# Optimization experiments

Measured on AMD Instinct MI355X. Metric: run time of the kernel, lower is better.

## Reference

```python
import jax, jax.numpy as jnp
import numpy as np

SIZES = (20, 20, 20, 20, 20)          # formula_oh_sizes
OH_N = sum(SIZES)                      # 100
NUM_BINS = 65536                       # spect_bin.get_num_bins()
EPS_SIZE = 1e-4                        # eps added to subset size
IN_EPS = 1e-5                          # torch InstanceNorm1d default eps


def thermometer_oh(counts):
    # StructuredOneHot with accum=True: per-element thermometer encoding.
    # counts: (N, E) element counts -> (N, sum(SIZES)) with out[j]=1 iff j < count.
    outs = [(jnp.arange(s, dtype=counts.dtype)[None, :] < counts[:, i:i + 1]).astype(jnp.float32)
            for i, s in enumerate(SIZES)]
    return jnp.concatenate(outs, axis=-1)


def inorm(x):
    # InstanceNorm1d (affine=False) as applied here: normalize over last dim per row.
    m = jnp.mean(x, axis=-1, keepdims=True)
    v = jnp.var(x, axis=-1, keepdims=True)
    return (x - m) * jax.lax.rsqrt(v + IN_EPS)


def _lin(key, fan_in, fan_out):
    k1, k2 = jax.random.split(key)
    bound = 1.0 / np.sqrt(fan_in)
    W = jax.random.uniform(k1, (fan_in, fan_out), jnp.float32, -bound, bound)
    b = jax.random.uniform(k2, (fan_out,), jnp.float32, -bound, bound)
    return W, b


def setup_inputs():
    key = jax.random.key(0)
    ks = jax.random.split(key, 12)
    B, A, GF, S, P, E, D = 8, 48, 256, 4096, 32, 5, 256
    vert_feat_in = jax.random.normal(ks[0], (B, A, GF), jnp.float32)
    vert_mask_in = jnp.ones((B, A), jnp.float32)
    elem_idx = jax.random.randint(ks[1], (B, A), 0, E)
    vert_element_oh = jax.nn.one_hot(elem_idx, E, dtype=jnp.float32)
    adj_oh = jnp.zeros((B, A, A), jnp.float32)                      # unused by forward path
    atom_subsets = jax.random.randint(ks[2], (B, S, A), 0, 2).astype(jnp.int32)
    atom_subsets_peaks = jnp.zeros((1,), jnp.float32)               # unused (mass_idx/intensity used)
    mass_idx = jax.random.randint(ks[3], (B, S, P), 0, NUM_BINS).astype(jnp.int32)
    intensity = jax.random.uniform(ks[4], (B, S, P), jnp.float32)
    combine_W, combine_b = _lin(ks[5], OH_N + GF, GF)
    l1_W, l1_b = _lin(ks[6], GF, D)
    l2a_W, l2a_b = _lin(ks[7], D, D)
    l2b_W, l2b_b = _lin(ks[8], D, D)
    score_W, score_b = _lin(ks[9], D, 1)
    return {
        'vert_feat_in': vert_feat_in, 'vert_mask_in': vert_mask_in,
        'vert_element_oh': vert_element_oh, 'adj_oh': adj_oh,
        'atom_subsets': atom_subsets, 'atom_subsets_peaks': atom_subsets_peaks,
        'mass_idx': mass_idx, 'intensity': intensity,
        'combine_W': combine_W, 'combine_b': combine_b,
        'l1_W': l1_W, 'l1_b': l1_b, 'l2a_W': l2a_W, 'l2a_b': l2a_b,
        'l2b_W': l2b_W, 'l2b_b': l2b_b, 'score_W': score_W, 'score_b': score_b,
    }


def reference(vert_feat_in, vert_mask_in, vert_element_oh, adj_oh, atom_subsets,
              atom_subsets_peaks, mass_idx, intensity,
              combine_W, combine_b, l1_W, l1_b, l2a_W, l2a_b, l2b_W, l2b_b,
              score_W, score_b):
    B, A, GF = vert_feat_in.shape
    _, S, _ = atom_subsets.shape
    subsets_f = atom_subsets.astype(jnp.float32)
    masked_vert = vert_feat_in * vert_mask_in[:, :, None]               # (B,A,GF)
    subsets_masked = subsets_f * vert_mask_in[:, None, :]               # (B,S,A)
    # weighted sum of vertex features over each subset
    sws = jnp.einsum('bag,bsa->bsg', masked_vert, subsets_masked)        # (B,S,GF)
    # per-subset element counts -> structured one-hot formula encoding
    counts = jnp.einsum('bae,bsa->bse', vert_element_oh, subsets_f)      # (B,S,E)
    pf_oh = thermometer_oh(counts.reshape(-1, counts.shape[-1])).reshape(B, S, OH_N)
    subset_size = jnp.sum(subsets_masked, axis=2) + EPS_SIZE             # (B,S)
    mean_feat = sws / subset_size[:, :, None]
    normed = inorm(mean_feat)                                            # subset_weighted_norm
    combined = jax.nn.relu(jnp.concatenate([pf_oh, normed], -1) @ combine_W + combine_b)
    x = inorm(combined)                                                  # norm_post_combine
    x = jax.nn.relu(x @ l1_W + l1_b)
    x = jax.nn.leaky_relu(x @ l2a_W + l2a_b)
    x = jax.nn.leaky_relu(x @ l2b_W + l2b_b)
    x = jax.nn.relu(x)
    x = inorm(x)                                                         # norm_pre_score
    scores = (x @ score_W + score_b)[..., 0]                             # (B,S)
    probs = jax.nn.softmax(scores, axis=-1)
    # per-batch sparse mass-matrix binning: scatter-add intensity*prob into spectral bins
    weighted = intensity * probs[:, :, None]                             # (B,S,P)
    seg = jax.vmap(lambda idx, w: jax.ops.segment_sum(w, idx, num_segments=NUM_BINS))
    spect_out = seg(mass_idx.reshape(B, -1), weighted.reshape(B, -1))    # (B,NUM_BINS)
    return spect_out, probs
```

## Files before the change

### kernel.cpp

```cpp
#include <hip/hip_runtime.h>
#include <math.h>

#define B_DIM 8
#define A_DIM 48
#define GF_DIM 256
#define S_DIM 4096
#define P_DIM 32
#define E_DIM 5
#define OHN 100
#define NBINS 65536

typedef __attribute__((ext_vector_type(8))) short short8v;
typedef __attribute__((ext_vector_type(4))) float float4v;

__device__ __forceinline__ float wave_sum(float v) {
#pragma unroll
    for (int o = 32; o; o >>= 1) v += __shfl_xor(v, o, 64);
    return v;
}
__device__ __forceinline__ float wave_max(float v) {
#pragma unroll
    for (int o = 32; o; o >>= 1) v = fmaxf(v, __shfl_xor(v, o, 64));
    return v;
}
__device__ __forceinline__ float quad16_sum(float v) {
    v += __shfl_xor(v, 1, 64); v += __shfl_xor(v, 2, 64);
    v += __shfl_xor(v, 4, 64); v += __shfl_xor(v, 8, 64);
    return v;
}
__device__ __forceinline__ unsigned short bf16_rn(float x) {
    unsigned int u = __float_as_uint(x);
    return (unsigned short)((u + 0x7FFFu + ((u >> 16) & 1u)) >> 16);
}
__device__ __forceinline__ float bf16_val(unsigned short h) {
    return __uint_as_float(((unsigned int)h) << 16);
}
__device__ __forceinline__ float4v mfma_bf16(short8v a, short8v b, float4v c) {
    return __builtin_amdgcn_mfma_f32_16x16x32_bf16(a, b, c, 0, 0, 0);
}

__global__ __launch_bounds__(256) void k_prep(
    const float* __restrict__ cW, const float* __restrict__ l1W,
    const float* __restrict__ l2aW, const float* __restrict__ l2bW,
    const float* __restrict__ vert_feat, const float* __restrict__ vert_mask,
    const float* __restrict__ elem_oh,
    short* __restrict__ wp, short* __restrict__ wv,
    float* __restrict__ maskB, int* __restrict__ eiB,
    float4* __restrict__ spect4)
{
    const int blk = blockIdx.x;
    const int tid = threadIdx.x;
    if (blk < 1152) {
        int e = blk * 256 + tid;
        int c = e >> 13;
        int i = e & 8191;
        int j    = i & 7;
        int lane = (i >> 3) & 63;
        int nt   = (i >> 9) & 1;
        int wn   = i >> 10;
        int krel = (lane >> 4) * 8 + j;
        int n    = wn * 32 + nt * 16 + (lane & 15);
        float val = 0.f;
        if (c < 12) {
            int kp = c * 32 + krel;
            if (kp < 100)       val = cW[kp * 256 + n];
            else if (kp >= 128) val = cW[(kp - 28) * 256 + n];
        } else {
            int L  = (c - 12) >> 3;
            int kc = (c - 12) & 7;
            const float* W = (L == 0) ? l1W : (L == 1) ? l2aW : l2bW;
            val = W[(kc * 32 + krel) * 256 + n];
        }
        unsigned short h = bf16_rn(val);
        float lo = val - bf16_val(h);
        int base = c * 16384 + (i & 511);
        wp[base + (wn * 4 + nt) * 512]     = (short)h;
        wp[base + (wn * 4 + 2 + nt) * 512] = (short)bf16_rn(lo);
    } else if (blk < 1664) {
        int vb = blk - 1152;
        int vc = vb >> 5;
        int i  = (vb & 31) * 256 + tid;
        int b  = vc >> 1, v = vc & 1;
        int j    = i & 7;
        int lane = (i >> 3) & 63;
        int nt   = (i >> 9) & 1;
        int wn   = i >> 10;
        int k = v * 32 + (lane >> 4) * 8 + j;
        int n = wn * 32 + nt * 16 + (lane & 15);
        float val = 0.f;
        if (k < A_DIM) {
            float mk = vert_mask[b * A_DIM + k];
            val = vert_feat[((size_t)(b * A_DIM + k)) * GF_DIM + n] * mk * mk;
        }
        unsigned short h = bf16_rn(val);
        float lo = val - bf16_val(h);
        int base = vc * 16384 + (i & 511);
        wv[base + (wn * 4 + nt) * 512]     = (short)h;
        wv[base + (wn * 4 + 2 + nt) * 512] = (short)bf16_rn(lo);
    } else if (blk == 1664) {
        for (int t = tid; t < B_DIM * A_DIM; t += 256) {
            maskB[t] = vert_mask[t];
            int ei = 0;
#pragma unroll
            for (int e = 0; e < E_DIM; ++e)
                if (elem_oh[t * E_DIM + e] > 0.5f) ei = e;
            eiB[t] = ei;
        }
    } else {
        int z = (blk - 1665) * 256 + tid;
        spect4[z] = make_float4(0.f, 0.f, 0.f, 0.f);
    }
}

#define L_XAL 16384
#define L_PS  32768
#define L_TM  34816
#define L_INV 35328
#define L_TOT 35456

template <int NKC, int ACT, bool NORM, bool SCORE, bool THERM>
__device__ __forceinline__ void layer_pass(
    short* xAh, short* xAl, float (*ps)[64], const uint4* __restrict__ tm,
    const short* __restrict__ wstream, const float* __restrict__ bias,
    const float* __restrict__ sW, const float* __restrict__ sb,
    float* __restrict__ scores, int R0)
{
    const int tid  = threadIdx.x;
    const int lane = tid & 63;
    const int wn   = tid >> 6;
    const int quad = lane >> 4;
    const int col  = lane & 15;
    const short* wbase = wstream + wn * 2048 + lane * 8;

    unsigned int tw01 = 0, tw23 = 0;
    if (THERM) {
        const int sh = quad * 8;
        uint4 t0 = tm[col];
        uint4 t1 = tm[16 + col];
        tw01 = ((t0.x >> sh) & 0xFFu)        | (((t1.x >> sh) & 0xFFu) << 8)
             | (((t0.y >> sh) & 0xFFu) << 16) | (((t1.y >> sh) & 0xFFu) << 24);
        tw23 = ((t0.z >> sh) & 0xFFu)        | (((t1.z >> sh) & 0xFFu) << 8)
             | (((t0.w >> sh) & 0xFFu) << 16) | (((t1.w >> sh) & 0xFFu) << 24);
    }

    float4v acc[2][2];
#pragma unroll
    for (int mi = 0; mi < 2; ++mi)
#pragma unroll
        for (int nt = 0; nt < 2; ++nt) acc[mi][nt] = (float4v){0.f, 0.f, 0.f, 0.f};

    short8v bh[2][2], bl[2][2];
    {
        const short* q = wbase;
        bh[0][0] = *(const short8v*)(q);
        bh[0][1] = *(const short8v*)(q + 512);
        bl[0][0] = *(const short8v*)(q + 1024);
        bl[0][1] = *(const short8v*)(q + 1536);
    }

#pragma unroll
    for (int kc = 0; kc < NKC; ++kc) {
        const int cur = kc & 1;
        if (kc + 1 < NKC) {
            const int nxt = (kc + 1) & 1;
            const short* q = wbase + (kc + 1) * 16384;
            bh[nxt][0] = *(const short8v*)(q);
            bh[nxt][1] = *(const short8v*)(q + 512);
            bl[nxt][0] = *(const short8v*)(q + 1024);
            bl[nxt][1] = *(const short8v*)(q + 1536);
        }
        const bool isT = THERM && (kc < 4);
        short8v ah[2], al[2];
        if (isT) {
            const unsigned int w = (kc < 2) ? tw01 : tw23;
#pragma unroll
            for (int mi = 0; mi < 2; ++mi) {
                const int bb = (kc & 1) * 16 + mi * 8;
                short8v hv;
#pragma unroll
                for (int j = 0; j < 8; ++j)
                    hv[j] = (short)(((w >> (bb + j)) & 1u) ? 0x3F80 : 0);
                ah[mi] = hv;
            }
        } else {
            const int ki = THERM ? (kc - 4) : kc;
#pragma unroll
            for (int mi = 0; mi < 2; ++mi) {
                ah[mi] = *(const short8v*)(xAh + ((ki * 2 + mi) * 64 + lane) * 8);
                al[mi] = *(const short8v*)(xAl + ((ki * 2 + mi) * 64 + lane) * 8);
            }
        }
#pragma unroll
        for (int mi = 0; mi < 2; ++mi)
#pragma unroll
            for (int nt = 0; nt < 2; ++nt) {
                acc[mi][nt] = mfma_bf16(ah[mi], bh[cur][nt], acc[mi][nt]);
                acc[mi][nt] = mfma_bf16(ah[mi], bl[cur][nt], acc[mi][nt]);
                if (!isT)
                    acc[mi][nt] = mfma_bf16(al[mi], bh[cur][nt], acc[mi][nt]);
            }
    }

    float bc0 = bias[wn * 32 + col];
    float bc1 = bias[wn * 32 + 16 + col];
#pragma unroll
    for (int mi = 0; mi < 2; ++mi)
#pragma unroll
        for (int r = 0; r < 4; ++r) {
            float z0 = acc[mi][0][r] + bc0;
            float z1 = acc[mi][1][r] + bc1;
            if (ACT == 0) { z0 = fmaxf(z0, 0.f); z1 = fmaxf(z1, 0.f); }
            else { z0 = (z0 > 0.f) ? z0 : 0.01f * z0; z1 = (z1 > 0.f) ? z1 : 0.01f * z1; }
            acc[mi][0][r] = z0; acc[mi][1][r] = z1;
        }

    __syncthreads();

    if (NORM) {
#pragma unroll
        for (int mi = 0; mi < 2; ++mi)
#pragma unroll
            for (int r = 0; r < 4; ++r) {
                float s  = acc[mi][0][r] + acc[mi][1][r];
                float s2 = acc[mi][0][r] * acc[mi][0][r]
                         + acc[mi][1][r] * acc[mi][1][r];
                s  = quad16_sum(s);
                s2 = quad16_sum(s2);
                if (col == 0) {
                    ps[wn][mi * 16 + quad * 4 + r]      = s;
                    ps[wn][32 + mi * 16 + quad * 4 + r] = s2;
                }
            }
        __syncthreads();
#pragma unroll
        for (int mi = 0; mi < 2; ++mi)
#pragma unroll
            for (int r = 0; r < 4; ++r) {
                int m = mi * 16 + quad * 4 + r;
                float s = 0.f, s2 = 0.f;
#pragma unroll
                for (int w = 0; w < 8; ++w) { s += ps[w][m]; s2 += ps[w][32 + m]; }
                float mean = s * (1.f / 256.f);
                float var  = s2 * (1.f / 256.f) - mean * mean;
                float rsf  = 1.0f / sqrtf(var + 1e-5f);
                acc[mi][0][r] = (acc[mi][0][r] - mean) * rsf;
                acc[mi][1][r] = (acc[mi][1][r] - mean) * rsf;
            }
    }

    if (SCORE) {
        __syncthreads();
        float sv0 = sW[wn * 32 + col];
        float sv1 = sW[wn * 32 + 16 + col];
        float psu[2][4];
#pragma unroll
        for (int mi = 0; mi < 2; ++mi)
#pragma unroll
            for (int r = 0; r < 4; ++r)
                psu[mi][r] = quad16_sum(acc[mi][0][r] * sv0 + acc[mi][1][r] * sv1);
        if (col == 0) {
#pragma unroll
            for (int mi = 0; mi < 2; ++mi)
#pragma unroll
                for (int r = 0; r < 4; ++r)
                    ps[wn][mi * 16 + quad * 4 + r] = psu[mi][r];
        }
        __syncthreads();
        if (tid < 32) {
            float s = sb[0];
#pragma unroll
            for (int w = 0; w < 8; ++w) s += ps[w][tid];
            scores[R0 + tid] = s;
        }
    } else {
#pragma unroll
        for (int mi = 0; mi < 2; ++mi)
#pragma unroll
            for (int nt = 0; nt < 2; ++nt) {
                int nn0 = (nt * 16 + col) & ~1;
                int q2  = nn0 >> 3;
                int j0  = nn0 & 7;
#pragma unroll
                for (int r = 0; r < 4; ++r) {
                    float v  = acc[mi][nt][r];
                    float pv = __shfl_xor(v, 1, 64);
                    int m15 = quad * 4 + r;
                    int rowidx = (wn * 2 + mi) * 64 + q2 * 16 + m15;
                    if ((col & 1) == 0) {
                        unsigned int wd = (unsigned int)bf16_rn(v)
                                        | ((unsigned int)bf16_rn(pv) << 16);
                        ((unsigned int*)xAh)[rowidx * 4 + (j0 >> 1)] = wd;
                    } else {
                        float ls = v  - bf16_val(bf16_rn(v));
                        float lp = pv - bf16_val(bf16_rn(pv));
                        unsigned int wd = (unsigned int)bf16_rn(lp)
                                        | ((unsigned int)bf16_rn(ls) << 16);
                        ((unsigned int*)xAl)[rowidx * 4 + (j0 >> 1)] = wd;
                    }
                }
            }
        __syncthreads();
    }
}

__global__ __launch_bounds__(512, 4) void k_mlp(
    const int* __restrict__ subsets, const short* __restrict__ wprep,
    const short* __restrict__ vertB,
    const float* __restrict__ maskB, const int* __restrict__ eiB,
    const float* __restrict__ cb,  const float* __restrict__ l1b,
    const float* __restrict__ l2ab, const float* __restrict__ l2bb,
    const float* __restrict__ sW,  const float* __restrict__ sb,
    float* __restrict__ scores)
{
    __shared__ __align__(16) char smem[L_TOT];
    short*  xAh = (short*)smem;
    short*  xAl = (short*)(smem + L_XAL);
    short*  fm  = (short*)(smem + L_XAL);
    float (*ps)[64]  = (float(*)[64])(smem + L_PS);
    uint4*  tm       = (uint4*)(smem + L_TM);
    float*  invsz    = (float*)(smem + L_INV);

    const int tid  = threadIdx.x;
    const int lane = tid & 63;
    const int wn   = tid >> 6;
    const int quad = lane >> 4;
    const int col  = lane & 15;
    const int fb   = blockIdx.x;
    const int b    = fb >> 7;
    const int R0   = fb * 32;

    if (tid < 256) {
        int g  = tid;
        int lg = g & 63;
        int t2 = g >> 6;
        int kc = t2 >> 1, mi = t2 & 1;
        int m  = mi * 16 + (lg & 15);
        int k0 = kc * 32 + (lg >> 4) * 8;
        const int* srow = subsets + (size_t)(R0 + m) * A_DIM;
        short8v hv;
#pragma unroll
        for (int j = 0; j < 8; ++j) {
            int k = k0 + j;
            hv[j] = (short)((k < A_DIM && srow[k]) ? 0x3F80 : 0);
        }
        *(short8v*)(fm + g * 8) = hv;
    }

    {
        const float mymask = (lane < A_DIM) ? maskB[b * A_DIM + lane] : 0.f;
        const int   myei   = (lane < A_DIM) ? eiB[b * A_DIM + lane]   : -1;
        unsigned long long* tmw = (unsigned long long*)tm;
#pragma unroll
        for (int i = 0; i < 4; ++i) {
            int r = wn * 4 + i;
            int fl = (lane < A_DIM) ? subsets[(size_t)(R0 + r) * A_DIM + lane] : 0;
            unsigned long long m0 = __ballot(fl != 0 && myei == 0);
            unsigned long long m1 = __ballot(fl != 0 && myei == 1);
            unsigned long long m2 = __ballot(fl != 0 && myei == 2);
            unsigned long long m3 = __ballot(fl != 0 && myei == 3);
            unsigned long long m4 = __ballot(fl != 0 && myei == 4);
            float ssz = wave_sum(fl ? mymask : 0.f) + 1e-4f;
            if (lane == 0) {
                unsigned int c0 = __popcll(m0), c1 = __popcll(m1),
                             c2 = __popcll(m2), c3 = __popcll(m3),
                             c4 = __popcll(m4);
                unsigned long long r0 = (1ull << (c0 > 20u ? 20u : c0)) - 1ull;
                unsigned long long r1 = (1ull << (c1 > 20u ? 20u : c1)) - 1ull;
                unsigned long long r2 = (1ull << (c2 > 20u ? 20u : c2)) - 1ull;
                unsigned long long r3 = (1ull << (c3 > 20u ? 20u : c3)) - 1ull;
                unsigned long long r4 = (1ull << (c4 > 20u ? 20u : c4)) - 1ull;
                unsigned long long lo = r0 | (r1 << 20) | (r2 << 40) | (r3 << 60);
                unsigned long long hi = (r3 >> 4) | (r4 << 16);
                tmw[r * 2]     = lo;
                tmw[r * 2 + 1] = hi;
                invsz[r]  = 1.0f / ssz;
            }
        }
    }
    __syncthreads();

    {
        const short* wbase = vertB + b * 32768 + wn * 2048 + lane * 8;
        float4v acc[2][2];
#pragma unroll
        for (int mi = 0; mi < 2; ++mi)
#pragma unroll
            for (int nt = 0; nt < 2; ++nt) acc[mi][nt] = (float4v){0.f, 0.f, 0.f, 0.f};

        short8v bh[2][2], bl[2][2];
#pragma unroll
        for (int kc = 0; kc < 2; ++kc) {
            const short* q = wbase + kc * 16384;
            bh[kc][0] = *(const short8v*)(q);
            bh[kc][1] = *(const short8v*)(q + 512);
            bl[kc][0] = *(const short8v*)(q + 1024);
            bl[kc][1] = *(const short8v*)(q + 1536);
        }
#pragma unroll
        for (int kc = 0; kc < 2; ++kc) {
            short8v a0 = *(const short8v*)(fm + ((kc * 2 + 0) * 64 + lane) * 8);
            short8v a1 = *(const short8v*)(fm + ((kc * 2 + 1) * 64 + lane) * 8);
#pragma unroll
            for (int nt = 0; nt < 2; ++nt) {
                acc[0][nt] = mfma_bf16(a0, bh[kc][nt], acc[0][nt]);
                acc[0][nt] = mfma_bf16(a0, bl[kc][nt], acc[0][nt]);
                acc[1][nt] = mfma_bf16(a1, bh[kc][nt], acc[1][nt]);
                acc[1][nt] = mfma_bf16(a1, bl[kc][nt], acc[1][nt]);
            }
        }

#pragma unroll
        for (int mi = 0; mi < 2; ++mi)
#pragma unroll
            for (int r = 0; r < 4; ++r) {
                float iv = invsz[mi * 16 + quad * 4 + r];
                acc[mi][0][r] *= iv;
                acc[mi][1][r] *= iv;
            }

        __syncthreads();

        {
#pragma unroll
            for (int mi = 0; mi < 2; ++mi)
#pragma unroll
                for (int r = 0; r < 4; ++r) {
                    float s  = acc[mi][0][r] + acc[mi][1][r];
                    float s2 = acc[mi][0][r] * acc[mi][0][r]
                             + acc[mi][1][r] * acc[mi][1][r];
                    s  = quad16_sum(s);
                    s2 = quad16_sum(s2);
                    if (col == 0) {
                        ps[wn][mi * 16 + quad * 4 + r]      = s;
                        ps[wn][32 + mi * 16 + quad * 4 + r] = s2;
                    }
                }
            __syncthreads();
#pragma unroll
            for (int mi = 0; mi < 2; ++mi)
#pragma unroll
                for (int r = 0; r < 4; ++r) {
                    int m = mi * 16 + quad * 4 + r;
                    float s = 0.f, s2 = 0.f;
#pragma unroll
                    for (int w = 0; w < 8; ++w) { s += ps[w][m]; s2 += ps[w][32 + m]; }
                    float mean = s * (1.f / 256.f);
                    float var  = s2 * (1.f / 256.f) - mean * mean;
                    float rsf  = 1.0f / sqrtf(var + 1e-5f);
                    acc[mi][0][r] = (acc[mi][0][r] - mean) * rsf;
                    acc[mi][1][r] = (acc[mi][1][r] - mean) * rsf;
                }
        }

#pragma unroll
        for (int mi = 0; mi < 2; ++mi)
#pragma unroll
            for (int nt = 0; nt < 2; ++nt) {
                int nn0 = (nt * 16 + col) & ~1;
                int q2  = nn0 >> 3;
                int j0  = nn0 & 7;
#pragma unroll
                for (int r = 0; r < 4; ++r) {
                    float v  = acc[mi][nt][r];
                    float pv = __shfl_xor(v, 1, 64);
                    int m15 = quad * 4 + r;
                    int rowidx = (wn * 2 + mi) * 64 + q2 * 16 + m15;
                    if ((col & 1) == 0) {
                        unsigned int wd = (unsigned int)bf16_rn(v)
                                        | ((unsigned int)bf16_rn(pv) << 16);
                        ((unsigned int*)xAh)[rowidx * 4 + (j0 >> 1)] = wd;
                    } else {
                        float ls = v  - bf16_val(bf16_rn(v));
                        float lp = pv - bf16_val(bf16_rn(pv));
                        unsigned int wd = (unsigned int)bf16_rn(lp)
                                        | ((unsigned int)bf16_rn(ls) << 16);
                        ((unsigned int*)xAl)[rowidx * 4 + (j0 >> 1)] = wd;
                    }
                }
            }
        __syncthreads();
    }

    layer_pass<12, 0, true,  false, true >(xAh, xAl, ps, tm, wprep,
        cb, nullptr, nullptr, nullptr, R0);
    layer_pass< 8, 0, false, false, false>(xAh, xAl, ps, tm, wprep + 12 * 16384,
        l1b, nullptr, nullptr, nullptr, R0);
    layer_pass< 8, 1, false, false, false>(xAh, xAl, ps, tm, wprep + 20 * 16384,
        l2ab, nullptr, nullptr, nullptr, R0);
    layer_pass< 8, 0, true,  true,  false>(xAh, xAl, ps, tm, wprep + 28 * 16384,
        l2bb, sW, sb, scores, R0);
}

__global__ __launch_bounds__(256) void k_softmax(float* __restrict__ probs) {
    const int b   = blockIdx.x;
    const int tid = threadIdx.x;
    __shared__ float redA[4];
    __shared__ float redB[4];
    float* sp = probs + (size_t)b * S_DIM;

    float v[16];
    float mx = -INFINITY;
#pragma unroll
    for (int i = 0; i < 16; ++i) {
        v[i] = sp[tid + i * 256];
        mx = fmaxf(mx, v[i]);
    }
    mx = wave_max(mx);
    if ((tid & 63) == 0) redA[tid >> 6] = mx;
    __syncthreads();
    mx = fmaxf(fmaxf(redA[0], redA[1]), fmaxf(redA[2], redA[3]));

    float sum = 0.f;
#pragma unroll
    for (int i = 0; i < 16; ++i) {
        v[i] = expf(v[i] - mx);
        sum += v[i];
    }
    sum = wave_sum(sum);
    if ((tid & 63) == 0) redB[tid >> 6] = sum;
    __syncthreads();
    float tot = redB[0] + redB[1] + redB[2] + redB[3];
    float inv = 1.0f / tot;
#pragma unroll
    for (int i = 0; i < 16; ++i) sp[tid + i * 256] = v[i] * inv;
}

__global__ __launch_bounds__(256) void k_scatter(
    const int*   __restrict__ mass_idx,
    const float* __restrict__ intensity,
    const float* __restrict__ probs,
    float* __restrict__ spect)
{
    int i  = blockIdx.x * 256 + threadIdx.x;
    int bs = i >> 5;
    int b  = i >> 17;
    float w = intensity[i] * probs[bs];
    unsafeAtomicAdd(spect + ((size_t)b << 16) + mass_idx[i], w);
}

extern "C" void kernel_launch(void* const* d_in, const int* in_sizes, int n_in,
                              void* d_out, int out_size, void* d_ws, size_t ws_size,
                              hipStream_t stream) {
    const float* vert_feat = (const float*)d_in[0];
    const float* vert_mask = (const float*)d_in[1];
    const float* elem_oh   = (const float*)d_in[2];
    const int*   subsets   = (const int*)d_in[4];
    const int*   mass_idx  = (const int*)d_in[6];
    const float* intensity = (const float*)d_in[7];
    const float* combine_W = (const float*)d_in[8];
    const float* combine_b = (const float*)d_in[9];
    const float* l1_W      = (const float*)d_in[10];
    const float* l1_b      = (const float*)d_in[11];
    const float* l2a_W     = (const float*)d_in[12];
    const float* l2a_b     = (const float*)d_in[13];
    const float* l2b_W     = (const float*)d_in[14];
    const float* l2b_b     = (const float*)d_in[15];
    const float* score_W   = (const float*)d_in[16];
    const float* score_b   = (const float*)d_in[17];

    float* out   = (float*)d_out;
    float* spect = out;
    float* probs = out + (size_t)B_DIM * NBINS;

    short* wprep = (short*)d_ws;
    short* vertB = wprep + 36 * 16384;
    float* maskB = (float*)(vertB + 16 * 16384);
    int*   eiB   = (int*)(maskB + B_DIM * A_DIM);

    k_prep<<<2177, 256, 0, stream>>>(combine_W, l1_W, l2a_W, l2b_W,
        vert_feat, vert_mask, elem_oh, wprep, vertB, maskB, eiB,
        (float4*)spect);
    k_mlp<<<1024, 512, 0, stream>>>(subsets, wprep, vertB, maskB, eiB,
        combine_b, l1_b, l2a_b, l2b_b, score_W, score_b, probs);
    k_softmax<<<B_DIM, 256, 0, stream>>>(probs);
    k_scatter<<<(B_DIM * S_DIM * P_DIM) / 256, 256, 0, stream>>>(
        mass_idx, intensity, probs, spect);
}
```

Before: 278.2 us.

## Deepen weight prefetch, split norm reductions, vectorize scatter loads

The MLP GEMM weight fragments are now prefetched two K-chunks ahead through a three-slot register ring instead of one chunk ahead, to hide more global-load latency at the cost of extra registers. The instance-norm sum and sum-of-squares reductions are split into separate loops, and the variance is clamped at zero. The scatter kernel now has each thread load four mass indices and intensities as int4/float4 and issue four atomics, using a quarter as many blocks. The deeper prefetch may raise register pressure and lower occupancy.

```diff
diff --git a/kernel.cpp b/kernel.cpp
--- a/kernel.cpp
+++ b/kernel.cpp
@@ -149,21 +149,24 @@
 #pragma unroll
         for (int nt = 0; nt < 2; ++nt) acc[mi][nt] = (float4v){0.f, 0.f, 0.f, 0.f};
 
-    short8v bh[2][2], bl[2][2];
-    {
-        const short* q = wbase;
-        bh[0][0] = *(const short8v*)(q);
-        bh[0][1] = *(const short8v*)(q + 512);
-        bl[0][0] = *(const short8v*)(q + 1024);
-        bl[0][1] = *(const short8v*)(q + 1536);
+    short8v bh[3][2], bl[3][2];
+#pragma unroll
+    for (int p = 0; p < 2; ++p) {
+        if (p < NKC) {
+            const short* q = wbase + p * 16384;
+            bh[p][0] = *(const short8v*)(q);
+            bh[p][1] = *(const short8v*)(q + 512);
+            bl[p][0] = *(const short8v*)(q + 1024);
+            bl[p][1] = *(const short8v*)(q + 1536);
+        }
     }
 
 #pragma unroll
     for (int kc = 0; kc < NKC; ++kc) {
-        const int cur = kc & 1;
-        if (kc + 1 < NKC) {
-            const int nxt = (kc + 1) & 1;
-            const short* q = wbase + (kc + 1) * 16384;
+        const int cur = kc % 3;
+        if (kc + 2 < NKC) {
+            const int nxt = (kc + 2) % 3;
+            const short* q = wbase + (kc + 2) * 16384;
             bh[nxt][0] = *(const short8v*)(q);
             bh[nxt][1] = *(const short8v*)(q + 512);
             bl[nxt][0] = *(const short8v*)(q + 1024);
@@ -221,15 +224,16 @@
         for (int mi = 0; mi < 2; ++mi)
 #pragma unroll
             for (int r = 0; r < 4; ++r) {
-                float s  = acc[mi][0][r] + acc[mi][1][r];
-                float s2 = acc[mi][0][r] * acc[mi][0][r]
-                         + acc[mi][1][r] * acc[mi][1][r];
-                s  = quad16_sum(s);
-                s2 = quad16_sum(s2);
-                if (col == 0) {
-                    ps[wn][mi * 16 + quad * 4 + r]      = s;
-                    ps[wn][32 + mi * 16 + quad * 4 + r] = s2;
-                }
+                float s = quad16_sum(acc[mi][0][r] + acc[mi][1][r]);
+                if (col == 0) ps[wn][mi * 16 + quad * 4 + r] = s;
+            }
+#pragma unroll
+        for (int mi = 0; mi < 2; ++mi)
+#pragma unroll
+            for (int r = 0; r < 4; ++r) {
+                float s2 = quad16_sum(acc[mi][0][r] * acc[mi][0][r]
+                                    + acc[mi][1][r] * acc[mi][1][r]);
+                if (col == 0) ps[wn][32 + mi * 16 + quad * 4 + r] = s2;
             }
         __syncthreads();
 #pragma unroll
@@ -241,7 +245,7 @@
 #pragma unroll
                 for (int w = 0; w < 8; ++w) { s += ps[w][m]; s2 += ps[w][32 + m]; }
                 float mean = s * (1.f / 256.f);
-                float var  = s2 * (1.f / 256.f) - mean * mean;
+                float var  = fmaxf(s2 * (1.f / 256.f) - mean * mean, 0.f);
                 float rsf  = 1.0f / sqrtf(var + 1e-5f);
                 acc[mi][0][r] = (acc[mi][0][r] - mean) * rsf;
                 acc[mi][1][r] = (acc[mi][1][r] - mean) * rsf;
@@ -425,15 +429,16 @@
             for (int mi = 0; mi < 2; ++mi)
 #pragma unroll
                 for (int r = 0; r < 4; ++r) {
-                    float s  = acc[mi][0][r] + acc[mi][1][r];
-                    float s2 = acc[mi][0][r] * acc[mi][0][r]
-                             + acc[mi][1][r] * acc[mi][1][r];
-                    s  = quad16_sum(s);
-                    s2 = quad16_sum(s2);
-                    if (col == 0) {
-                        ps[wn][mi * 16 + quad * 4 + r]      = s;
-                        ps[wn][32 + mi * 16 + quad * 4 + r] = s2;
-                    }
+                    float s = quad16_sum(acc[mi][0][r] + acc[mi][1][r]);
+                    if (col == 0) ps[wn][mi * 16 + quad * 4 + r] = s;
+                }
+#pragma unroll
+            for (int mi = 0; mi < 2; ++mi)
+#pragma unroll
+                for (int r = 0; r < 4; ++r) {
+                    float s2 = quad16_sum(acc[mi][0][r] * acc[mi][0][r]
+                                        + acc[mi][1][r] * acc[mi][1][r]);
+                    if (col == 0) ps[wn][32 + mi * 16 + quad * 4 + r] = s2;
                 }
             __syncthreads();
 #pragma unroll
@@ -445,7 +450,7 @@
 #pragma unroll
                     for (int w = 0; w < 8; ++w) { s += ps[w][m]; s2 += ps[w][32 + m]; }
                     float mean = s * (1.f / 256.f);
-                    float var  = s2 * (1.f / 256.f) - mean * mean;
+                    float var  = fmaxf(s2 * (1.f / 256.f) - mean * mean, 0.f);
                     float rsf  = 1.0f / sqrtf(var + 1e-5f);
                     acc[mi][0][r] = (acc[mi][0][r] - mean) * rsf;
                     acc[mi][1][r] = (acc[mi][1][r] - mean) * rsf;
@@ -531,11 +536,18 @@
     const float* __restrict__ probs,
     float* __restrict__ spect)
 {
-    int i  = blockIdx.x * 256 + threadIdx.x;
+    int g  = blockIdx.x * 256 + threadIdx.x;
+    int i  = g << 2;
     int bs = i >> 5;
     int b  = i >> 17;
-    float w = intensity[i] * probs[bs];
-    unsafeAtomicAdd(spect + ((size_t)b << 16) + mass_idx[i], w);
+    float p = probs[bs];
+    int4   m4 = *(const int4*)(mass_idx + i);
+    float4 w4 = *(const float4*)(intensity + i);
+    float* sb = spect + ((size_t)b << 16);
+    unsafeAtomicAdd(sb + m4.x, w4.x * p);
+    unsafeAtomicAdd(sb + m4.y, w4.y * p);
+    unsafeAtomicAdd(sb + m4.z, w4.z * p);
+    unsafeAtomicAdd(sb + m4.w, w4.w * p);
 }
 
 extern "C" void kernel_launch(void* const* d_in, const int* in_sizes, int n_in,
@@ -573,6 +585,6 @@
     k_mlp<<<1024, 512, 0, stream>>>(subsets, wprep, vertB, maskB, eiB,
         combine_b, l1_b, l2a_b, l2b_b, score_W, score_b, probs);
     k_softmax<<<B_DIM, 256, 0, stream>>>(probs);
-    k_scatter<<<(B_DIM * S_DIM * P_DIM) / 256, 256, 0, stream>>>(
+    k_scatter<<<(B_DIM * S_DIM * P_DIM) / (256 * 4), 256, 0, stream>>>(
         mass_idx, intensity, probs, spect);
 }
```

Result: slower. 289.5 us (+4.1%).
